# Performance work log

Hardware: AMD Instinct MI355X
Metric: run time of the kernel (lower is better)

## Reference

```python
import jax, jax.numpy as jnp
import numpy as np

N = 100000   # nodes
E = 1600000  # edges (avg degree 16)
D = 128      # feature dim (in_size == out_size)
L = 3        # n_layers

def setup_inputs() -> dict:
    key = jax.random.key(0)
    k0, k1, k2, k3, k4 = jax.random.split(key, 5)
    x = jax.random.normal(k0, (N, D), dtype=jnp.float32)
    src = jax.random.randint(k1, (E,), 0, N)
    dst = jax.random.randint(k2, (E,), 0, N)
    # positive edge weights (DGL EdgeWeightNorm requires nonnegative)
    edge_weight = jax.random.uniform(k3, (E,), dtype=jnp.float32) + 0.1
    W = jax.random.normal(k4, (L, D, D), dtype=jnp.float32) / np.float32(np.sqrt(D))
    b = jnp.zeros((L, D), dtype=jnp.float32)
    return {"x": x, "edge_weight": edge_weight, "W": W, "b": b, "src": src, "dst": dst}

def reference(x, edge_weight, W, b, src, dst):
    n = x.shape[0]
    # EdgeWeightNorm(norm='both'): w_ij / sqrt(deg_out_w(src_i) * deg_in_w(dst_j))
    deg_src = jax.ops.segment_sum(edge_weight, src, num_segments=n)  # weighted out-degree
    deg_dst = jax.ops.segment_sum(edge_weight, dst, num_segments=n)  # weighted in-degree
    nw = edge_weight * jax.lax.rsqrt(deg_src[src] * deg_dst[dst])    # [E]
    h = x
    for i in range(W.shape[0]):
        # GraphConv(norm='none'): transform, weighted-sum aggregate, bias, ELU
        h = h @ W[i]                                   # [N, D]
        msg = h[src] * nw[:, None]                     # [E, D] gather + scale
        h = jax.ops.segment_sum(msg, dst, num_segments=n) + b[i]
        h = jax.nn.elu(h)
    return h
```

## Files before the change

### kernel.cpp

```cpp
#include <hip/hip_runtime.h>
#include <hip/hip_bf16.h>


#define D128 128
#define PBLK 256
#define BUCKET_SHIFT 8
#define DCAP 7168

typedef __attribute__((ext_vector_type(8))) short s8v;
typedef __attribute__((ext_vector_type(16))) float f16v;

__device__ __forceinline__ float elu1(float x) {
    return x > 0.f ? x : (expf(x) - 1.f);
}

__device__ __forceinline__ unsigned short bf16_rne(float v) {
    unsigned u = __float_as_uint(v);
    return (unsigned short)((u + 0x7fffu + ((u >> 16) & 1u)) >> 16);
}


__global__ __launch_bounds__(256) void part_hist2(
    const int* __restrict__ src, const int* __restrict__ dst,
    int* __restrict__ histT2, int E, int nb, int chunk, int hlen) {
    extern __shared__ int sh[];
    for (int i = threadIdx.x; i < 2 * nb; i += 256) sh[i] = 0;
    __syncthreads();
    int b = blockIdx.x;
    int beg = b * chunk, end = min(E, beg + chunk);
    for (int e = beg + threadIdx.x; e < end; e += 256) {
        atomicAdd(&sh[dst[e] >> BUCKET_SHIFT], 1);
        atomicAdd(&sh[nb + (src[e] >> BUCKET_SHIFT)], 1);
    }
    __syncthreads();
    for (int i = threadIdx.x; i < nb; i += 256)
        histT2[i * PBLK + b] = sh[i];
    for (int i = threadIdx.x; i < nb; i += 256)
        histT2[hlen + i * PBLK + b] = sh[nb + i];
}

__global__ __launch_bounds__(256) void scan_block(
    int* __restrict__ data, int* __restrict__ blockSums, int n) {
    __shared__ int tmp[256];
    int gid = blockIdx.x * 256 + threadIdx.x;
    int v = (gid < n) ? data[gid] : 0;
    tmp[threadIdx.x] = v;
    __syncthreads();
    for (int off = 1; off < 256; off <<= 1) {
        int t = (threadIdx.x >= off) ? tmp[threadIdx.x - off] : 0;
        __syncthreads();
        tmp[threadIdx.x] += t;
        __syncthreads();
    }
    if (gid < n) data[gid] = tmp[threadIdx.x] - v;
    if (threadIdx.x == 255) blockSums[blockIdx.x] = tmp[255];
}

__global__ __launch_bounds__(1024) void scan_sums(int* __restrict__ bsums, int nb) {
    __shared__ int tmp[1024];
    int v = (threadIdx.x < nb) ? bsums[threadIdx.x] : 0;
    tmp[threadIdx.x] = v;
    __syncthreads();
    for (int off = 1; off < 1024; off <<= 1) {
        int t = (threadIdx.x >= off) ? tmp[threadIdx.x - off] : 0;
        __syncthreads();
        tmp[threadIdx.x] += t;
        __syncthreads();
    }
    if (threadIdx.x < nb) bsums[threadIdx.x] = tmp[threadIdx.x] - v;
}

__global__ __launch_bounds__(256) void part_scatter2(
    const int* __restrict__ src, const int* __restrict__ dst,
    const float* __restrict__ w, const int* __restrict__ offsT2,
    const int* __restrict__ bsums,
    int2* __restrict__ pkw, int2* __restrict__ skw,
    int E, int nb, int chunk, int hlen) {
    extern __shared__ int cur[];
    int b = blockIdx.x;
    for (int i = threadIdx.x; i < nb; i += 256)
        cur[i] = offsT2[i * PBLK + b] + bsums[i];
    for (int i = threadIdx.x; i < nb; i += 256)
        cur[nb + i] = offsT2[hlen + i * PBLK + b] + bsums[nb + i] - E;
    __syncthreads();
    int beg = b * chunk, end = min(E, beg + chunk);
    for (int e = beg + threadIdx.x; e < end; e += 256) {
        int d = dst[e];
        int s = src[e];
        int wv = __float_as_int(w[e]);
        int kd = d >> BUCKET_SHIFT;
        int pos = atomicAdd(&cur[kd], 1);
        pkw[pos] = make_int2((int)((unsigned)s | ((unsigned)(d & 255) << 24)), wv);
        int ks = s >> BUCKET_SHIFT;
        int posS = atomicAdd(&cur[nb + ks], 1);
        skw[posS] = make_int2(s & 255, wv);
    }
}

__global__ __launch_bounds__(256) void bucket_sumS(
    const int2* __restrict__ skw, const int* __restrict__ offsT2,
    const int* __restrict__ bsums,
    float* __restrict__ deg_src, int E, int nb, int N, int hlen) {
    __shared__ float wsum[256];
    int k = blockIdx.x;
    int base = offsT2[hlen + k * PBLK] + bsums[nb + k] - E;
    int end = (k + 1 < nb) ? (offsT2[hlen + (k + 1) * PBLK] + bsums[nb + k + 1] - E) : E;
    int t = threadIdx.x;
    wsum[t] = 0.f;
    __syncthreads();
    for (int i = base + t; i < end; i += 256) {
        int2 v = skw[i];
        atomicAdd(&wsum[v.x], __int_as_float(v.y));
    }
    __syncthreads();
    int node = (k << BUCKET_SHIFT) + t;
    if (node < N) deg_src[node] = wsum[t];
}

__global__ __launch_bounds__(256) void bucket_build(
    const int2* __restrict__ pkw, const int* __restrict__ offsT,
    const int* __restrict__ bsums, const float* __restrict__ deg_src,
    int* __restrict__ row_start, int2* __restrict__ edata,
    int E, int nb, int N) {
    __shared__ int cnt[256];
    __shared__ float wsum[256];
    __shared__ int loc[256];
    __shared__ int cur2[256];
    extern __shared__ int2 stage[];

    int k = blockIdx.x;
    int base = offsT[k * PBLK] + bsums[k];
    int end = (k + 1 < nb) ? (offsT[(k + 1) * PBLK] + bsums[k + 1]) : E;
    int m = end - base;
    int t = threadIdx.x;
    cnt[t] = 0;
    wsum[t] = 0.f;
    __syncthreads();
    bool staged = (m <= DCAP);
    for (int i = t; i < m; i += 256) {
        int2 kw = pkw[base + i];
        if (staged) stage[i] = kw;
        int dl = (unsigned)kw.x >> 24;
        atomicAdd(&cnt[dl], 1);
        atomicAdd(&wsum[dl], __int_as_float(kw.y));
    }
    __syncthreads();
    int v = cnt[t];
    loc[t] = v;
    __syncthreads();
    for (int off = 1; off < 256; off <<= 1) {
        int tv = (t >= off) ? loc[t - off] : 0;
        __syncthreads();
        loc[t] += tv;
        __syncthreads();
    }
    int excl = loc[t] - v;
    loc[t] = excl;
    cur2[t] = 0;
    int node = (k << BUCKET_SHIFT) + t;
    if (node < N) row_start[node] = base + excl;
    if (k == 0 && t == 0) row_start[N] = E;
    __syncthreads();
    for (int i = t; i < m; i += 256) {
        int2 kw = staged ? stage[i] : pkw[base + i];
        int dl = (unsigned)kw.x >> 24;
        int s = kw.x & 0xFFFFFF;
        int pos = base + loc[dl] + atomicAdd(&cur2[dl], 1);
        float nw = __int_as_float(kw.y) * rsqrtf(deg_src[s] * wsum[dl]);
        edata[pos] = make_int2(s << 8, __float_as_int(nw));
    }
}


__global__ __launch_bounds__(256) void prep_w(
    const float* __restrict__ W, unsigned short* __restrict__ Wh,
    unsigned short* __restrict__ Wl, int total) {
    int i = blockIdx.x * 256 + threadIdx.x;
    if (i >= total) return;
    int l = i >> 14;
    int rem = i & 16383;
    int k = rem >> 7, nn = rem & 127;
    float v = W[i];
    unsigned short h = bf16_rne(v);
    float fh = __uint_as_float((unsigned)h << 16);
    unsigned short lo = bf16_rne(v - fh);
    size_t oi = ((((size_t)l * 16 + (k >> 3)) * 128 + nn) << 3) + (k & 7);
    Wh[oi] = h;
    Wl[oi] = lo;
}

__global__ __launch_bounds__(256) void gemm_mfma_f32(
    const float* __restrict__ A, const unsigned short* __restrict__ Wh,
    const unsigned short* __restrict__ Wl, unsigned short* __restrict__ Hb,
    int n, int nblk) {
    __shared__ s8v lds_hi[16][32];
    __shared__ s8v lds_lo[16][32];
    const int t = threadIdx.x;
    const int l = t & 63;
    const int wv = t >> 6;
    const int n0 = wv * 32;
    const int lr = l & 31, lh = l >> 5;

    s8v bh[8], bl[8];
#pragma unroll
    for (int k0 = 0; k0 < 8; ++k0) {
        int kc = k0 * 2 + lh;
        size_t gi = ((size_t)kc * 128 + n0 + lr) << 3;
        bh[k0] = *(const s8v*)(Wh + gi);
        bl[k0] = *(const s8v*)(Wl + gi);
    }

    const int row = t >> 3;
    const int kc0 = t & 7;
    for (int rb = blockIdx.x; rb < nblk; rb += gridDim.x) {
        const int r0 = rb * 32;
        __syncthreads();
        {
            int r = r0 + row;
#pragma unroll
            for (int hhalf = 0; hhalf < 2; ++hhalf) {
                int kc = kc0 + 8 * hhalf;
                float4 v0 = make_float4(0.f, 0.f, 0.f, 0.f), v1 = v0;
                if (r < n) {
                    const float4* ap = (const float4*)(A + (size_t)r * D128 + kc * 8);
                    v0 = ap[0];
                    v1 = ap[1];
                }
                s8v sh, sl;
#pragma unroll
                for (int e = 0; e < 8; ++e) {
                    float v = (e < 4) ? ((const float*)&v0)[e] : ((const float*)&v1)[e - 4];
                    unsigned short h = bf16_rne(v);
                    float fh = __uint_as_float((unsigned)h << 16);
                    sh[e] = (short)h;
                    sl[e] = (short)bf16_rne(v - fh);
                }
                lds_hi[kc][row ^ (kc & 7)] = sh;
                lds_lo[kc][row ^ (kc & 7)] = sl;
            }
        }
        __syncthreads();

        f16v acc = {0.f, 0.f, 0.f, 0.f, 0.f, 0.f, 0.f, 0.f,
                    0.f, 0.f, 0.f, 0.f, 0.f, 0.f, 0.f, 0.f};
#pragma unroll
        for (int k0 = 0; k0 < 8; ++k0) {
            int kc = k0 * 2 + lh;
            s8v ah = lds_hi[kc][lr ^ (kc & 7)];
            s8v al = lds_lo[kc][lr ^ (kc & 7)];
            acc = __builtin_amdgcn_mfma_f32_32x32x16_bf16(ah, bh[k0], acc, 0, 0, 0);
            acc = __builtin_amdgcn_mfma_f32_32x32x16_bf16(ah, bl[k0], acc, 0, 0, 0);
            acc = __builtin_amdgcn_mfma_f32_32x32x16_bf16(al, bh[k0], acc, 0, 0, 0);
        }

#pragma unroll
        for (int rg = 0; rg < 16; ++rg) {
            int grow = r0 + (rg & 3) + 8 * (rg >> 2) + 4 * lh;
            if (grow < n) Hb[(size_t)grow * D128 + n0 + lr] = bf16_rne(acc[rg]);
        }
    }
}

__global__ __launch_bounds__(256) void gemm_mfma_bf16(
    const unsigned short* __restrict__ A, const unsigned short* __restrict__ Wh,
    const unsigned short* __restrict__ Wl, unsigned short* __restrict__ Hb,
    int n, int nblk) {
    __shared__ s8v lds_a[16][64];
    const int t = threadIdx.x;
    const int l = t & 63;
    const int wv = t >> 6;
    const int n0 = wv * 32;
    const int lr = l & 31, lh = l >> 5;

    s8v bh[8], bl[8];
#pragma unroll
    for (int k0 = 0; k0 < 8; ++k0) {
        int kc = k0 * 2 + lh;
        size_t gi = ((size_t)kc * 128 + n0 + lr) << 3;
        bh[k0] = *(const s8v*)(Wh + gi);
        bl[k0] = *(const s8v*)(Wl + gi);
    }

    for (int rb = blockIdx.x; rb < nblk; rb += gridDim.x) {
        const int r0 = rb * 64;
        __syncthreads();
#pragma unroll
        for (int g4 = 0; g4 < 4; ++g4) {
            int g = t * 4 + g4;
            int row = g >> 4, kc = g & 15;
            int r = r0 + row;
            s8v v = {0, 0, 0, 0, 0, 0, 0, 0};
            if (r < n) v = *(const s8v*)(A + (size_t)r * D128 + kc * 8);
            lds_a[kc][row ^ (kc & 7)] = v;
        }
        __syncthreads();

        f16v acc0 = {0.f, 0.f, 0.f, 0.f, 0.f, 0.f, 0.f, 0.f,
                     0.f, 0.f, 0.f, 0.f, 0.f, 0.f, 0.f, 0.f};
        f16v acc1 = acc0;
#pragma unroll
        for (int k0 = 0; k0 < 8; ++k0) {
            int kc = k0 * 2 + lh;
            s8v a0 = lds_a[kc][lr ^ (kc & 7)];
            s8v a1 = lds_a[kc][(32 + lr) ^ (kc & 7)];
            acc0 = __builtin_amdgcn_mfma_f32_32x32x16_bf16(a0, bh[k0], acc0, 0, 0, 0);
            acc0 = __builtin_amdgcn_mfma_f32_32x32x16_bf16(a0, bl[k0], acc0, 0, 0, 0);
            acc1 = __builtin_amdgcn_mfma_f32_32x32x16_bf16(a1, bh[k0], acc1, 0, 0, 0);
            acc1 = __builtin_amdgcn_mfma_f32_32x32x16_bf16(a1, bl[k0], acc1, 0, 0, 0);
        }

#pragma unroll
        for (int rg = 0; rg < 16; ++rg) {
            int rr = (rg & 3) + 8 * (rg >> 2) + 4 * lh;
            int grow0 = r0 + rr;
            int grow1 = r0 + 32 + rr;
            if (grow0 < n) Hb[(size_t)grow0 * D128 + n0 + lr] = bf16_rne(acc0[rg]);
            if (grow1 < n) Hb[(size_t)grow1 * D128 + n0 + lr] = bf16_rne(acc1[rg]);
        }
    }
}


__global__ __launch_bounds__(256) void aggregate_bf16(
    const unsigned short* __restrict__ hb, const int* __restrict__ rs,
    const int2* __restrict__ edata, const float* __restrict__ bias,
    unsigned short* __restrict__ outb, float* __restrict__ outf,
    int obf, int n) {
    int wave = threadIdx.x >> 6;
    int lane = threadIdx.x & 63;
    int node = blockIdx.x * 8 + wave * 2 + (lane >> 5);
    if (node >= n) return;
    int beg = rs[node], end = rs[node + 1];
    int eg = (lane >> 4) & 1;
    int c = lane & 15;
    const char* base = (const char*)hb + c * 16;
    float a0[8] = {0.f, 0.f, 0.f, 0.f, 0.f, 0.f, 0.f, 0.f};
    float a1[8] = {0.f, 0.f, 0.f, 0.f, 0.f, 0.f, 0.f, 0.f};
    int i = beg;
    for (; i + 3 < end; i += 4) {
        int2 e0 = edata[i + eg];
        int2 e1 = edata[i + 2 + eg];
        uint4 p0 = *(const uint4*)(base + (unsigned)e0.x);
        uint4 p1 = *(const uint4*)(base + (unsigned)e1.x);
        float w0 = __int_as_float(e0.y), w1 = __int_as_float(e1.y);
#pragma unroll
        for (int j = 0; j < 4; ++j) {
            unsigned q0 = ((const unsigned*)&p0)[j];
            unsigned q1 = ((const unsigned*)&p1)[j];
            a0[2 * j]     = fmaf(__uint_as_float(q0 << 16), w0, a0[2 * j]);
            a0[2 * j + 1] = fmaf(__uint_as_float(q0 & 0xffff0000u), w0, a0[2 * j + 1]);
            a1[2 * j]     = fmaf(__uint_as_float(q1 << 16), w1, a1[2 * j]);
            a1[2 * j + 1] = fmaf(__uint_as_float(q1 & 0xffff0000u), w1, a1[2 * j + 1]);
        }
    }
    for (; i + eg < end; i += 2) {
        int2 e0 = edata[i + eg];
        uint4 p0 = *(const uint4*)(base + (unsigned)e0.x);
        float w0 = __int_as_float(e0.y);
#pragma unroll
        for (int j = 0; j < 4; ++j) {
            unsigned q0 = ((const unsigned*)&p0)[j];
            a0[2 * j]     = fmaf(__uint_as_float(q0 << 16), w0, a0[2 * j]);
            a0[2 * j + 1] = fmaf(__uint_as_float(q0 & 0xffff0000u), w0, a0[2 * j + 1]);
        }
    }
#pragma unroll
    for (int k = 0; k < 8; ++k) {
        a0[k] += a1[k];
        a0[k] += __shfl_xor(a0[k], 16);
    }
    if ((lane & 16) == 0) {
        float4 b0 = ((const float4*)bias)[c * 2];
        float4 b1 = ((const float4*)bias)[c * 2 + 1];
        float o[8];
        o[0] = elu1(a0[0] + b0.x);
        o[1] = elu1(a0[1] + b0.y);
        o[2] = elu1(a0[2] + b0.z);
        o[3] = elu1(a0[3] + b0.w);
        o[4] = elu1(a0[4] + b1.x);
        o[5] = elu1(a0[5] + b1.y);
        o[6] = elu1(a0[6] + b1.z);
        o[7] = elu1(a0[7] + b1.w);
        if (obf) {
            uint4 p;
            p.x = (unsigned)bf16_rne(o[0]) | ((unsigned)bf16_rne(o[1]) << 16);
            p.y = (unsigned)bf16_rne(o[2]) | ((unsigned)bf16_rne(o[3]) << 16);
            p.z = (unsigned)bf16_rne(o[4]) | ((unsigned)bf16_rne(o[5]) << 16);
            p.w = (unsigned)bf16_rne(o[6]) | ((unsigned)bf16_rne(o[7]) << 16);
            ((uint4*)(outb + (size_t)node * D128))[c] = p;
        } else {
            float4 q0 = make_float4(o[0], o[1], o[2], o[3]);
            float4 q1 = make_float4(o[4], o[5], o[6], o[7]);
            ((float4*)(outf + (size_t)node * D128))[c * 2] = q0;
            ((float4*)(outf + (size_t)node * D128))[c * 2 + 1] = q1;
        }
    }
}

extern "C" void kernel_launch(void* const* d_in, const int* in_sizes, int n_in,
                              void* d_out, int out_size, void* d_ws, size_t ws_size,
                              hipStream_t stream) {
    const float* x   = (const float*)d_in[0];
    const float* ew  = (const float*)d_in[1];
    const float* W   = (const float*)d_in[2];
    const float* b   = (const float*)d_in[3];
    const int*   src = (const int*)d_in[4];
    const int*   dst = (const int*)d_in[5];
    float* out = (float*)d_out;

    const int N = in_sizes[0] / D128;
    const int E = in_sizes[1];
    const int L = in_sizes[2] / (D128 * D128);
    const int nb = (N + 255) >> BUCKET_SHIFT;
    const int hlen = nb * PBLK;

    char* ws = (char*)d_ws;
    size_t off = 0;
    auto take = [&](size_t bytes) {
        void* p = ws + off;
        off = (off + bytes + 255) & ~(size_t)255;
        return p;
    };
    float* deg_src = (float*)take((size_t)N * 4);
    int*   histT2  = (int*)take((size_t)2 * hlen * 4);
    int*   bsums   = (int*)take(1024 * 4);
    int*   rstart  = (int*)take((size_t)(N + 1) * 4);
    int2*  edata   = (int2*)take((size_t)E * 8);
    unsigned short* Hb = (unsigned short*)take((size_t)N * D128 * 2);
    unsigned short* Ab = (unsigned short*)take((size_t)N * D128 * 2);
    unsigned short* Whg = (unsigned short*)take((size_t)L * D128 * D128 * 2);
    unsigned short* Wlg = (unsigned short*)take((size_t)L * D128 * D128 * 2);
    int2* pkw = (int2*)Ab;
    int2* skw = ((int2*)Ab) + E;

    const int chunk = (E + PBLK - 1) / PBLK;
    const int sb2 = (2 * hlen + 255) / 256;
    const size_t part_lds = (size_t)2 * nb * 4;
    const size_t dcap_lds = (size_t)DCAP * 8;

    const int wtotal = L * D128 * D128;
    prep_w<<<(wtotal + 255) / 256, 256, 0, stream>>>(W, Whg, Wlg, wtotal);

    part_hist2<<<PBLK, 256, part_lds, stream>>>(src, dst, histT2, E, nb, chunk, hlen);
    scan_block<<<sb2, 256, 0, stream>>>(histT2, bsums, 2 * hlen);
    scan_sums<<<1, 1024, 0, stream>>>(bsums, sb2);
    part_scatter2<<<PBLK, 256, part_lds, stream>>>(src, dst, ew, histT2, bsums,
                                                   pkw, skw, E, nb, chunk, hlen);
    bucket_sumS<<<nb, 256, 0, stream>>>(skw, histT2, bsums, deg_src, E, nb, N, hlen);
    bucket_build<<<nb, 256, dcap_lds, stream>>>(pkw, histT2, bsums, deg_src,
                                                rstart, edata, E, nb, N);

    const int t32 = (N + 31) / 32;
    const int t64 = (N + 63) / 64;
    const int gemm_grid = 512;
    const int agg_grid = (N + 7) / 8;

    gemm_mfma_f32<<<gemm_grid, 256, 0, stream>>>(x, Whg, Wlg, Hb, N, t32);
    aggregate_bf16<<<agg_grid, 256, 0, stream>>>(Hb, rstart, edata, b,
                                                 Ab, nullptr, 1, N);
    gemm_mfma_bf16<<<gemm_grid, 256, 0, stream>>>(Ab, Whg + D128 * D128,
                                                  Wlg + D128 * D128, Hb, N, t64);
    aggregate_bf16<<<agg_grid, 256, 0, stream>>>(Hb, rstart, edata, b + D128,
                                                 Ab, nullptr, 1, N);
    gemm_mfma_bf16<<<gemm_grid, 256, 0, stream>>>(Ab, Whg + 2 * D128 * D128,
                                                  Wlg + 2 * D128 * D128, Hb, N, t64);
    aggregate_bf16<<<agg_grid, 256, 0, stream>>>(Hb, rstart, edata, b + 2 * D128,
                                                 nullptr, out, 0, N);
}
```

Measured before the change: 340.9 us.

## Load GEMM A-operands directly from global memory and launch one block per tile

The two MFMA GEMM kernels no longer stage the activation tile through shared memory with barriers. Each lane now loads its MFMA A-fragment straight from global memory into registers, and the f32 path splits into hi/lo bf16 in registers. The persistent grid-stride loop of 512 blocks becomes one block per row tile, which removes the syncthreads and LDS traffic. In exchange, all four waves in a block redundantly load the same A rows from global (relying on cache), use more registers, and pay the per-block cost of reloading the weights.

New measurement: 364.1 us. 6.8% more time.

```diff
diff --git a/kernel.cpp b/kernel.cpp
--- a/kernel.cpp
+++ b/kernel.cpp
@@ -192,14 +192,13 @@
 __global__ __launch_bounds__(256) void gemm_mfma_f32(
     const float* __restrict__ A, const unsigned short* __restrict__ Wh,
     const unsigned short* __restrict__ Wl, unsigned short* __restrict__ Hb,
-    int n, int nblk) {
-    __shared__ s8v lds_hi[16][32];
-    __shared__ s8v lds_lo[16][32];
+    int n) {
     const int t = threadIdx.x;
     const int l = t & 63;
     const int wv = t >> 6;
     const int n0 = wv * 32;
     const int lr = l & 31, lh = l >> 5;
+    const int r0 = blockIdx.x * 32;
 
     s8v bh[8], bl[8];
 #pragma unroll
@@ -210,67 +209,53 @@
         bl[k0] = *(const s8v*)(Wl + gi);
     }
 
-    const int row = t >> 3;
-    const int kc0 = t & 7;
-    for (int rb = blockIdx.x; rb < nblk; rb += gridDim.x) {
-        const int r0 = rb * 32;
-        __syncthreads();
-        {
-            int r = r0 + row;
-#pragma unroll
-            for (int hhalf = 0; hhalf < 2; ++hhalf) {
-                int kc = kc0 + 8 * hhalf;
-                float4 v0 = make_float4(0.f, 0.f, 0.f, 0.f), v1 = v0;
-                if (r < n) {
-                    const float4* ap = (const float4*)(A + (size_t)r * D128 + kc * 8);
-                    v0 = ap[0];
-                    v1 = ap[1];
-                }
-                s8v sh, sl;
-#pragma unroll
-                for (int e = 0; e < 8; ++e) {
-                    float v = (e < 4) ? ((const float*)&v0)[e] : ((const float*)&v1)[e - 4];
-                    unsigned short h = bf16_rne(v);
-                    float fh = __uint_as_float((unsigned)h << 16);
-                    sh[e] = (short)h;
-                    sl[e] = (short)bf16_rne(v - fh);
-                }
-                lds_hi[kc][row ^ (kc & 7)] = sh;
-                lds_lo[kc][row ^ (kc & 7)] = sl;
-            }
+    int r = r0 + lr;
+    if (r >= n) r = n - 1;
+    const float4* pa = (const float4*)(A + (size_t)r * D128 + lh * 8);
+
+    float4 va[8][2];
+#pragma unroll
+    for (int k0 = 0; k0 < 8; ++k0) {
+        va[k0][0] = pa[k0 * 4];
+        va[k0][1] = pa[k0 * 4 + 1];
+    }
+
+    f16v acc = {0.f, 0.f, 0.f, 0.f, 0.f, 0.f, 0.f, 0.f,
+                0.f, 0.f, 0.f, 0.f, 0.f, 0.f, 0.f, 0.f};
+#pragma unroll
+    for (int k0 = 0; k0 < 8; ++k0) {
+        s8v ah, al;
+#pragma unroll
+        for (int e = 0; e < 8; ++e) {
+            float v = (e < 4) ? ((const float*)&va[k0][0])[e]
+                              : ((const float*)&va[k0][1])[e - 4];
+            unsigned short h = bf16_rne(v);
+            float fh = __uint_as_float((unsigned)h << 16);
+            ah[e] = (short)h;
+            al[e] = (short)bf16_rne(v - fh);
         }
-        __syncthreads();
-
-        f16v acc = {0.f, 0.f, 0.f, 0.f, 0.f, 0.f, 0.f, 0.f,
-                    0.f, 0.f, 0.f, 0.f, 0.f, 0.f, 0.f, 0.f};
-#pragma unroll
-        for (int k0 = 0; k0 < 8; ++k0) {
-            int kc = k0 * 2 + lh;
-            s8v ah = lds_hi[kc][lr ^ (kc & 7)];
-            s8v al = lds_lo[kc][lr ^ (kc & 7)];
-            acc = __builtin_amdgcn_mfma_f32_32x32x16_bf16(ah, bh[k0], acc, 0, 0, 0);
-            acc = __builtin_amdgcn_mfma_f32_32x32x16_bf16(ah, bl[k0], acc, 0, 0, 0);
-            acc = __builtin_amdgcn_mfma_f32_32x32x16_bf16(al, bh[k0], acc, 0, 0, 0);
-        }
-
-#pragma unroll
-        for (int rg = 0; rg < 16; ++rg) {
-            int grow = r0 + (rg & 3) + 8 * (rg >> 2) + 4 * lh;
-            if (grow < n) Hb[(size_t)grow * D128 + n0 + lr] = bf16_rne(acc[rg]);
-        }
+        acc = __builtin_amdgcn_mfma_f32_32x32x16_bf16(ah, bh[k0], acc, 0, 0, 0);
+        acc = __builtin_amdgcn_mfma_f32_32x32x16_bf16(ah, bl[k0], acc, 0, 0, 0);
+        acc = __builtin_amdgcn_mfma_f32_32x32x16_bf16(al, bh[k0], acc, 0, 0, 0);
+    }
+
+#pragma unroll
+    for (int rg = 0; rg < 16; ++rg) {
+        int grow = r0 + (rg & 3) + 8 * (rg >> 2) + 4 * lh;
+        if (grow < n) Hb[(size_t)grow * D128 + n0 + lr] = bf16_rne(acc[rg]);
     }
 }
 
 __global__ __launch_bounds__(256) void gemm_mfma_bf16(
     const unsigned short* __restrict__ A, const unsigned short* __restrict__ Wh,
     const unsigned short* __restrict__ Wl, unsigned short* __restrict__ Hb,
-    int n, int nblk) {
-    __shared__ s8v lds_a[16][64];
+    int n) {
     const int t = threadIdx.x;
     const int l = t & 63;
     const int wv = t >> 6;
     const int n0 = wv * 32;
     const int lr = l & 31, lh = l >> 5;
+    const int r0 = blockIdx.x * 64;
 
     s8v bh[8], bl[8];
 #pragma unroll
@@ -281,42 +266,38 @@
         bl[k0] = *(const s8v*)(Wl + gi);
     }
 
-    for (int rb = blockIdx.x; rb < nblk; rb += gridDim.x) {
-        const int r0 = rb * 64;
-        __syncthreads();
-#pragma unroll
-        for (int g4 = 0; g4 < 4; ++g4) {
-            int g = t * 4 + g4;
-            int row = g >> 4, kc = g & 15;
-            int r = r0 + row;
-            s8v v = {0, 0, 0, 0, 0, 0, 0, 0};
-            if (r < n) v = *(const s8v*)(A + (size_t)r * D128 + kc * 8);
-            lds_a[kc][row ^ (kc & 7)] = v;
-        }
-        __syncthreads();
-
-        f16v acc0 = {0.f, 0.f, 0.f, 0.f, 0.f, 0.f, 0.f, 0.f,
-                     0.f, 0.f, 0.f, 0.f, 0.f, 0.f, 0.f, 0.f};
-        f16v acc1 = acc0;
-#pragma unroll
-        for (int k0 = 0; k0 < 8; ++k0) {
-            int kc = k0 * 2 + lh;
-            s8v a0 = lds_a[kc][lr ^ (kc & 7)];
-            s8v a1 = lds_a[kc][(32 + lr) ^ (kc & 7)];
-            acc0 = __builtin_amdgcn_mfma_f32_32x32x16_bf16(a0, bh[k0], acc0, 0, 0, 0);
-            acc0 = __builtin_amdgcn_mfma_f32_32x32x16_bf16(a0, bl[k0], acc0, 0, 0, 0);
-            acc1 = __builtin_amdgcn_mfma_f32_32x32x16_bf16(a1, bh[k0], acc1, 0, 0, 0);
-            acc1 = __builtin_amdgcn_mfma_f32_32x32x16_bf16(a1, bl[k0], acc1, 0, 0, 0);
-        }
-
-#pragma unroll
-        for (int rg = 0; rg < 16; ++rg) {
-            int rr = (rg & 3) + 8 * (rg >> 2) + 4 * lh;
-            int grow0 = r0 + rr;
-            int grow1 = r0 + 32 + rr;
-            if (grow0 < n) Hb[(size_t)grow0 * D128 + n0 + lr] = bf16_rne(acc0[rg]);
-            if (grow1 < n) Hb[(size_t)grow1 * D128 + n0 + lr] = bf16_rne(acc1[rg]);
-        }
+    int ra = r0 + lr;
+    int rb2 = r0 + 32 + lr;
+    if (ra >= n) ra = n - 1;
+    if (rb2 >= n) rb2 = n - 1;
+    const s8v* pa0 = (const s8v*)(A + (size_t)ra * D128 + lh * 8);
+    const s8v* pa1 = (const s8v*)(A + (size_t)rb2 * D128 + lh * 8);
+
+    s8v a0[8], a1[8];
+#pragma unroll
+    for (int k0 = 0; k0 < 8; ++k0) {
+        a0[k0] = pa0[k0 * 2];
+        a1[k0] = pa1[k0 * 2];
+    }
+
+    f16v acc0 = {0.f, 0.f, 0.f, 0.f, 0.f, 0.f, 0.f, 0.f,
+                 0.f, 0.f, 0.f, 0.f, 0.f, 0.f, 0.f, 0.f};
+    f16v acc1 = acc0;
+#pragma unroll
+    for (int k0 = 0; k0 < 8; ++k0) {
+        acc0 = __builtin_amdgcn_mfma_f32_32x32x16_bf16(a0[k0], bh[k0], acc0, 0, 0, 0);
+        acc0 = __builtin_amdgcn_mfma_f32_32x32x16_bf16(a0[k0], bl[k0], acc0, 0, 0, 0);
+        acc1 = __builtin_amdgcn_mfma_f32_32x32x16_bf16(a1[k0], bh[k0], acc1, 0, 0, 0);
+        acc1 = __builtin_amdgcn_mfma_f32_32x32x16_bf16(a1[k0], bl[k0], acc1, 0, 0, 0);
+    }
+
+#pragma unroll
+    for (int rg = 0; rg < 16; ++rg) {
+        int rr = (rg & 3) + 8 * (rg >> 2) + 4 * lh;
+        int grow0 = r0 + rr;
+        int grow1 = r0 + 32 + rr;
+        if (grow0 < n) Hb[(size_t)grow0 * D128 + n0 + lr] = bf16_rne(acc0[rg]);
+        if (grow1 < n) Hb[(size_t)grow1 * D128 + n0 + lr] = bf16_rne(acc1[rg]);
     }
 }
 
@@ -450,20 +431,19 @@
     bucket_build<<<nb, 256, dcap_lds, stream>>>(pkw, histT2, bsums, deg_src,
                                                 rstart, edata, E, nb, N);
 
-    const int t32 = (N + 31) / 32;
-    const int t64 = (N + 63) / 64;
-    const int gemm_grid = 512;
+    const int g32 = (N + 31) / 32;
+    const int g64 = (N + 63) / 64;
     const int agg_grid = (N + 7) / 8;
 
-    gemm_mfma_f32<<<gemm_grid, 256, 0, stream>>>(x, Whg, Wlg, Hb, N, t32);
+    gemm_mfma_f32<<<g32, 256, 0, stream>>>(x, Whg, Wlg, Hb, N);
     aggregate_bf16<<<agg_grid, 256, 0, stream>>>(Hb, rstart, edata, b,
                                                  Ab, nullptr, 1, N);
-    gemm_mfma_bf16<<<gemm_grid, 256, 0, stream>>>(Ab, Whg + D128 * D128,
-                                                  Wlg + D128 * D128, Hb, N, t64);
+    gemm_mfma_bf16<<<g64, 256, 0, stream>>>(Ab, Whg + D128 * D128,
+                                            Wlg + D128 * D128, Hb, N);
     aggregate_bf16<<<agg_grid, 256, 0, stream>>>(Hb, rstart, edata, b + D128,
                                                  Ab, nullptr, 1, N);
-    gemm_mfma_bf16<<<gemm_grid, 256, 0, stream>>>(Ab, Whg + 2 * D128 * D128,
-                                                  Wlg + 2 * D128 * D128, Hb, N, t64);
+    gemm_mfma_bf16<<<g64, 256, 0, stream>>>(Ab, Whg + 2 * D128 * D128,
+                                            Wlg + 2 * D128 * D128, Hb, N);
     aggregate_bf16<<<agg_grid, 256, 0, stream>>>(Hb, rstart, edata, b + 2 * D128,
                                                  nullptr, out, 0, N);
 }
```
